# Kernel tuning notes

Measured on AMD Instinct MI355X. Metric: run time of the kernel, lower is better.

The kernel has to match this reference:

```python
import jax, jax.numpy as jnp
import numpy as np

D_MODEL = 5120
NUM_HEADS = 128
HEAD_DIM = D_MODEL // NUM_HEADS  # 40
LATENT = 1536


def setup_inputs() -> dict:
    key = jax.random.key(0)
    ks = jax.random.split(key, 9)
    B, S = 2, 1024
    scale = 0.02
    return {
        "x": jax.random.normal(ks[0], (B, S, D_MODEL), dtype=jnp.float32),
        "Wq": jax.random.normal(ks[1], (D_MODEL, D_MODEL), dtype=jnp.float32) * scale,
        "bq": jnp.zeros((D_MODEL,), dtype=jnp.float32),
        "Wc": jax.random.normal(ks[2], (D_MODEL, LATENT), dtype=jnp.float32) * scale,
        "bc": jnp.zeros((LATENT,), dtype=jnp.float32),
        "Wk": jax.random.normal(ks[3], (LATENT, D_MODEL), dtype=jnp.float32) * scale,
        "bk": jnp.zeros((D_MODEL,), dtype=jnp.float32),
        "Wv": jax.random.normal(ks[4], (LATENT, D_MODEL), dtype=jnp.float32) * scale,
        "bv": jnp.zeros((D_MODEL,), dtype=jnp.float32),
    }


def reference(x, Wq, bq, Wc, bc, Wk, bk, Wv, bv):
    B, S, _ = x.shape
    H, Dh = NUM_HEADS, HEAD_DIM
    # projections
    q = x @ Wq + bq                     # [B,S,D]
    kv_latent = x @ Wc + bc             # [B,S,L]
    k = kv_latent @ Wk + bk             # [B,S,D]
    v = kv_latent @ Wv + bv             # [B,S,D]
    # split heads -> [B,H,S,Dh]
    q = q.reshape(B, S, H, Dh).transpose(0, 2, 1, 3)
    k = k.reshape(B, S, H, Dh).transpose(0, 2, 1, 3)
    v = v.reshape(B, S, H, Dh).transpose(0, 2, 1, 3)
    scores = jnp.einsum("bhqd,bhkd->bhqk", q, k) / jnp.sqrt(jnp.float32(Dh))
    attn = jax.nn.softmax(scores, axis=-1)
    out = jnp.einsum("bhqk,bhkd->bhqd", attn, v)  # [B,H,S,Dh]
    return out.transpose(0, 2, 1, 3).reshape(B, S, H * Dh)
```

## Files before the change

kernel.cpp:

```cpp
#include <hip/hip_runtime.h>
#include <hip/hip_bf16.h>

typedef __attribute__((ext_vector_type(8))) __bf16 bf16x8;
typedef __attribute__((ext_vector_type(4))) __bf16 bf16x4;
typedef __attribute__((ext_vector_type(4))) float f32x4;

#define MFMA16(a, b, c) __builtin_amdgcn_mfma_f32_16x16x32_bf16((a), (b), (c), 0, 0, 0)

#if __has_builtin(__builtin_amdgcn_exp2f)
#define EXP2F(x) __builtin_amdgcn_exp2f(x)
#else
#define EXP2F(x) exp2f(x)
#endif

#define GLDS16(g, l)                                                             \
    __builtin_amdgcn_global_load_lds((const __attribute__((address_space(1))) void*)(g), \
                                     (__attribute__((address_space(3))) void*)(l), 16, 0, 0)

#define BARRIER()                          \
    do {                                   \
        asm volatile("" ::: "memory");     \
        __builtin_amdgcn_s_barrier();      \
        asm volatile("" ::: "memory");     \
    } while (0)

#define WAIT_LGKM0() asm volatile("s_waitcnt lgkmcnt(0)" ::: "memory")
#define VM6 asm volatile("s_waitcnt vmcnt(6)" ::: "memory")
#define VM8 asm volatile("s_waitcnt vmcnt(8)" ::: "memory")
#define VM0 asm volatile("s_waitcnt vmcnt(0)" ::: "memory")
#define VMNONE ((void)0)
#define KEEP(x) x
#define DROP(x)

static __device__ __forceinline__ unsigned short cvt_bf(float f) {
    return __builtin_bit_cast(unsigned short, (__bf16)f);
}

static __device__ __forceinline__ bf16x8 bf8_zero() {
    uint4 z = make_uint4(0, 0, 0, 0);
    return __builtin_bit_cast(bf16x8, z);
}

__global__ __launch_bounds__(256) void prep(const float* __restrict__ X,
                                            const float* __restrict__ Wq,
                                            const float* __restrict__ Wc,
                                            const float* __restrict__ Wk,
                                            const float* __restrict__ Wv,
                                            unsigned short* __restrict__ Xb,
                                            unsigned short* __restrict__ dqc,
                                            unsigned short* __restrict__ dkv) {
    const int D = 5120, L = 1536;
    int b = blockIdx.x, t = threadIdx.x;
    if (b < 5120) {
        int i = (b * 256 + t) * 8;
        float4 f0 = *(const float4*)(X + i);
        float4 f1 = *(const float4*)(X + i + 4);
        unsigned short o[8];
        o[0] = cvt_bf(f0.x); o[1] = cvt_bf(f0.y); o[2] = cvt_bf(f0.z); o[3] = cvt_bf(f0.w);
        o[4] = cvt_bf(f1.x); o[5] = cvt_bf(f1.y); o[6] = cvt_bf(f1.z); o[7] = cvt_bf(f1.w);
        *(uint4*)(Xb + i) = *(const uint4*)o;
        return;
    }
    int b2 = b - 5120;
    const float* W;
    unsigned short* WT;
    int K, N;
    if (b2 < 6400) { W = Wq; WT = dqc; K = D; N = D; }
    else if (b2 < 8320) { b2 -= 6400; W = Wc; WT = dqc + (size_t)D * D; K = D; N = L; }
    else if (b2 < 10240) { b2 -= 8320; W = Wk; WT = dkv; K = L; N = D; }
    else { b2 -= 10240; W = Wv; WT = dkv + (size_t)D * L; K = L; N = D; }
    int nx = N / 64;
    int n0 = (b2 % nx) * 64, k0 = (b2 / nx) * 64;

    __shared__ unsigned short tile[64][65];
    int c4 = (t & 15) * 4, r16 = t >> 4;
#pragma unroll
    for (int it = 0; it < 4; ++it) {
        int r = r16 + it * 16;
        float4 f = *(const float4*)&W[(size_t)(k0 + r) * N + n0 + c4];
        tile[r][c4 + 0] = cvt_bf(f.x);
        tile[r][c4 + 1] = cvt_bf(f.y);
        tile[r][c4 + 2] = cvt_bf(f.z);
        tile[r][c4 + 3] = cvt_bf(f.w);
    }
    __syncthreads();
    int n = t >> 2, kc = (t & 3) * 16;
    unsigned short o[16];
#pragma unroll
    for (int j = 0; j < 16; ++j) o[j] = tile[kc + j][n];
    unsigned short* dst = &WT[(size_t)(n0 + n) * K + k0 + kc];
    *(uint4*)dst = *(const uint4*)o;
    *(uint4*)(dst + 8) = *(const uint4*)(o + 8);
}

__global__ __launch_bounds__(256) void vtrans(const unsigned short* __restrict__ V, int ldv,
                                              unsigned short* __restrict__ VT) {
    int d0 = blockIdx.x * 64, s0 = blockIdx.y * 64;
    __shared__ __align__(16) unsigned short tile[64][72];
    int t = threadIdx.x;
    int r = t >> 3, c8 = (t & 7) * 8;
#pragma unroll
    for (int p = 0; p < 2; ++p) {
        uint4 u = *(const uint4*)&V[(size_t)(s0 + r + p * 32) * ldv + d0 + c8];
        *(uint4*)&tile[r + p * 32][c8] = u;
    }
    __syncthreads();
#pragma unroll
    for (int p = 0; p < 2; ++p) {
        int dr = (t >> 3) + p * 32, cc = (t & 7) * 8;
        unsigned short o[8];
#pragma unroll
        for (int j = 0; j < 8; ++j) o[j] = tile[cc + j][dr];
        *(uint4*)&VT[(size_t)(d0 + dr) * 2048 + s0 + cc] = *(const uint4*)o;
    }
}

#define STAGE_A(S, H, KT)                                                              \
    do {                                                                               \
        GLDS16(aS[H][0] + (size_t)(KT) * 64, &Abuf[S][(H) * 8192 + wid * 512]);        \
        GLDS16(aS[H][1] + (size_t)(KT) * 64, &Abuf[S][(H) * 8192 + 4096 + wid * 512]); \
    } while (0)
#define STAGE_B(S, H, KT)                                                              \
    do {                                                                               \
        GLDS16(bS[H][0] + (size_t)(KT) * 64, &Bbuf[S][(H) * 8192 + wid * 512]);        \
        GLDS16(bS[H][1] + (size_t)(KT) * 64, &Bbuf[S][(H) * 8192 + 4096 + wid * 512]); \
    } while (0)

#define LDA_HALF(S, QM)                                                                   \
    do {                                                                                  \
        _Pragma("unroll") for (int mi = 0; mi < 4; ++mi)                                  \
            _Pragma("unroll") for (int kh = 0; kh < 2; ++kh)                              \
                af[mi][kh] =                                                              \
                    *(const bf16x8*)&Abuf[S][((QM) * 8192 + aoff + mi * 1024) ^ (kh * 32)]; \
    } while (0)
#define LDB_HALF(S, QN, BF)                                                               \
    do {                                                                                  \
        _Pragma("unroll") for (int ni = 0; ni < 2; ++ni)                                  \
            _Pragma("unroll") for (int kh = 0; kh < 2; ++kh)                              \
                BF[ni][kh] =                                                              \
                    *(const bf16x8*)&Bbuf[S][((QN) * 8192 + boff + ni * 1024) ^ (kh * 32)]; \
    } while (0)

#define MMAQ(QM, QN, BF)                                                                \
    do {                                                                                \
        _Pragma("unroll") for (int mi = 0; mi < 4; ++mi)                                \
            _Pragma("unroll") for (int ni = 0; ni < 2; ++ni)                            \
                _Pragma("unroll") for (int kh = 0; kh < 2; ++kh)                        \
                    acc[(QM) * 4 + mi][(QN) * 2 + ni] =                                 \
                        MFMA16(af[mi][kh], BF[ni][kh], acc[(QM) * 4 + mi][(QN) * 2 + ni]); \
    } while (0)

#define KTILE_V2(S, T, STG1, STG2, VMOP, RDNEXT)       \
    {                                                  \
        const int s_ = (S);                            \
        LDB_HALF(s_, 1, bf1);                          \
        STG1(STAGE_B(s_ ^ 1, 0, (T) + 1);)             \
        __builtin_amdgcn_s_setprio(1);                 \
        MMAQ(0, 0, bf0);                               \
        __builtin_amdgcn_s_setprio(0);                 \
        WAIT_LGKM0();                                  \
        BARRIER();                                     \
        STG2(STAGE_A(s_, 0, (T) + 2);                  \
             STAGE_B(s_, 1, (T) + 2);)                 \
        __builtin_amdgcn_s_setprio(1);                 \
        MMAQ(0, 1, bf1);                               \
        __builtin_amdgcn_s_setprio(0);                 \
        LDA_HALF(s_, 1);                               \
        __builtin_amdgcn_s_setprio(1);                 \
        MMAQ(1, 1, bf1);                               \
        __builtin_amdgcn_s_setprio(0);                 \
        WAIT_LGKM0();                                  \
        BARRIER();                                     \
        STG2(STAGE_A(s_, 1, (T) + 2);)                 \
        __builtin_amdgcn_s_setprio(1);                 \
        MMAQ(1, 0, bf0);                               \
        __builtin_amdgcn_s_setprio(0);                 \
        VMOP;                                          \
        BARRIER();                                     \
        RDNEXT(LDA_HALF(s_ ^ 1, 0); LDB_HALF(s_ ^ 1, 0, bf0);) \
    }

__global__ __launch_bounds__(512, 2) void gemm256(const unsigned short* __restrict__ A, int lda,
                                                  const unsigned short* __restrict__ BT, int ldb,
                                                  const float* __restrict__ bias0,
                                                  const float* __restrict__ bias1, int nsplit,
                                                  unsigned short* __restrict__ C, int ldc,
                                                  int K, float s0, float s1, int gx) {
    __shared__ __align__(16) unsigned short Abuf[2][16384];
    __shared__ __align__(16) unsigned short Bbuf[2][16384];

    int nwg = gridDim.x, orig = blockIdx.x;
    int cpx = nwg >> 3;
    int wgid = (orig & 7) * cpx + (orig >> 3);
    int tm = wgid / gx, tn = wgid % gx;
    int m0 = tm * 256, n0 = tn * 256;

    int tid = threadIdx.x, lane = tid & 63, wid = tid >> 6;
    int wm = wid >> 2, wn = wid & 3;
    int lrow = lane & 15, lkg = lane >> 4;

    int t5 = tid >> 3;
    int cole = ((tid & 7) ^ ((tid >> 3) & 7)) << 3;
    const unsigned short* aS[2][2];
    const unsigned short* bS[2][2];
#pragma unroll
    for (int H = 0; H < 2; ++H)
#pragma unroll
        for (int c = 0; c < 2; ++c) {
            int rA = (c << 7) | (H << 6) | t5;
            int rB = (((c << 1) | (t5 >> 5)) << 6) | (H << 5) | (t5 & 31);
            aS[H][c] = A + (size_t)(m0 + rA) * lda + cole;
            bS[H][c] = BT + (size_t)(n0 + rB) * ldb + cole;
        }

    int xorc = (lkg * 8) ^ ((lrow & 7) << 3);
    int aoff = wm * 4096 + lrow * 64 + xorc;
    int boff = wn * 2048 + lrow * 64 + xorc;

    f32x4 acc[8][4];
#pragma unroll
    for (int i = 0; i < 8; ++i)
#pragma unroll
        for (int j = 0; j < 4; ++j) acc[i][j] = (f32x4){0.f, 0.f, 0.f, 0.f};
    bf16x8 af[4][2], bf0[2][2], bf1[2][2];

    const int nkt = K >> 6;

    STAGE_A(0, 0, 0); STAGE_A(0, 1, 0); STAGE_B(0, 0, 0); STAGE_B(0, 1, 0);
    STAGE_A(1, 0, 1); STAGE_B(1, 1, 1); STAGE_A(1, 1, 1);
    VM6;
    BARRIER();
    LDA_HALF(0, 0);
    LDB_HALF(0, 0, bf0);

    int t = 0;
    for (; t + 2 < nkt; ++t) KTILE_V2(t & 1, t, KEEP, KEEP, VM6, KEEP);
    KTILE_V2(t & 1, t, KEEP, DROP, VM0, KEEP);
    ++t;
    KTILE_V2(t & 1, t, DROP, DROP, VMNONE, DROP);

#pragma unroll
    for (int ni = 0; ni < 4; ++ni) {
        int col = n0 + wn * 64 + ni * 16 + lrow;
        float bval = (col < nsplit) ? bias0[col] : bias1[col - nsplit];
        float scl = (col < nsplit) ? s0 : s1;
#pragma unroll
        for (int mi = 0; mi < 8; ++mi) {
            int row = m0 + wm * 128 + mi * 16 + lkg * 4;
#pragma unroll
            for (int j = 0; j < 4; ++j)
                C[(size_t)(row + j) * ldc + col] = cvt_bf((acc[mi][ni][j] + bval) * scl);
        }
    }
}

#define STG128(S, KT)                                                                  \
    do {                                                                               \
        _Pragma("unroll") for (int i_ = 0; i_ < 4; ++i_)                               \
            GLDS16(Ag + (size_t)(i_ * 32) * lda + (size_t)(KT) * 64,                   \
                   &Abuf[S][i_ * 2048 + wid * 512]);                                   \
        _Pragma("unroll") for (int i_ = 0; i_ < 4; ++i_)                               \
            GLDS16(Bg + (size_t)(i_ * 32) * ldb + (size_t)(KT) * 64,                   \
                   &Bbuf[S][i_ * 2048 + wid * 512]);                                   \
    } while (0)

__global__ __launch_bounds__(256, 2) void gemm128(const unsigned short* __restrict__ A, int lda,
                                                  const unsigned short* __restrict__ BT, int ldb,
                                                  const float* __restrict__ bias0,
                                                  const float* __restrict__ bias1, int nsplit,
                                                  unsigned short* __restrict__ C, int ldc,
                                                  int K, float s0, float s1, int gy) {
    __shared__ __align__(16) unsigned short Abuf[2][8192];
    __shared__ __align__(16) unsigned short Bbuf[2][8192];

    int b = blockIdx.x;
    int tm = b % gy, tn = b / gy;
    int m0 = tm * 128, n0 = tn * 128;
    int tid = threadIdx.x, lane = tid & 63, wid = tid >> 6;
    int wm = wid >> 1, wn = wid & 1;
    int lrow = lane & 15, lkg = lane >> 4;

    int srow = tid >> 3;
    int cole = ((tid & 7) ^ ((tid >> 3) & 7)) << 3;
    const unsigned short* Ag = A + (size_t)(m0 + srow) * lda + cole;
    const unsigned short* Bg = BT + (size_t)(n0 + srow) * ldb + cole;

    int xorc8 = (lrow & 7) << 3;
    int aoff = (wm * 64 + lrow) * 64;
    int boff = (wn * 64 + lrow) * 64;

    f32x4 acc[4][4];
#pragma unroll
    for (int i2 = 0; i2 < 4; ++i2)
#pragma unroll
        for (int j = 0; j < 4; ++j) acc[i2][j] = (f32x4){0.f, 0.f, 0.f, 0.f};

    const int nkt = K >> 6;
    STG128(0, 0);
    for (int t = 0; t < nkt; ++t) {
        const int cur = t & 1;
        if (t + 1 < nkt) {
            STG128(cur ^ 1, t + 1);
            VM8;
        } else {
            VM0;
        }
        BARRIER();
        bf16x8 af[4][2], bv[4][2];
#pragma unroll
        for (int mi = 0; mi < 4; ++mi)
#pragma unroll
            for (int kh = 0; kh < 2; ++kh)
                af[mi][kh] = *(const bf16x8*)&Abuf[cur][aoff + mi * 1024 + (((kh * 4 + lkg) << 3) ^ xorc8)];
#pragma unroll
        for (int ni = 0; ni < 4; ++ni)
#pragma unroll
            for (int kh = 0; kh < 2; ++kh)
                bv[ni][kh] = *(const bf16x8*)&Bbuf[cur][boff + ni * 1024 + (((kh * 4 + lkg) << 3) ^ xorc8)];
        __builtin_amdgcn_s_setprio(1);
#pragma unroll
        for (int mi = 0; mi < 4; ++mi)
#pragma unroll
            for (int ni = 0; ni < 4; ++ni)
#pragma unroll
                for (int kh = 0; kh < 2; ++kh)
                    acc[mi][ni] = MFMA16(af[mi][kh], bv[ni][kh], acc[mi][ni]);
        __builtin_amdgcn_s_setprio(0);
        BARRIER();
    }

#pragma unroll
    for (int ni = 0; ni < 4; ++ni) {
        int col = n0 + wn * 64 + ni * 16 + lrow;
        float bval = (col < nsplit) ? bias0[col] : bias1[col - nsplit];
        float scl = (col < nsplit) ? s0 : s1;
#pragma unroll
        for (int mi = 0; mi < 4; ++mi) {
            int row = m0 + wm * 64 + mi * 16 + lkg * 4;
#pragma unroll
            for (int j = 0; j < 4; ++j)
                C[(size_t)(row + j) * ldc + col] = cvt_bf((acc[mi][ni][j] + bval) * scl);
        }
    }
}

__global__ __launch_bounds__(256) void attn(const unsigned short* __restrict__ q, int ldq,
                                            const unsigned short* __restrict__ k, int ldk,
                                            const unsigned short* __restrict__ vT,
                                            float* __restrict__ out) {
    const int S = 1024, D = 5120, Dh = 40;
    int b = blockIdx.z, h = blockIdx.y, qt = blockIdx.x;
    int t = threadIdx.x, lane = t & 63, wid = t >> 6;
    int lrow = lane & 15, lkg = lane >> 4;

    __shared__ __align__(16) unsigned short Ks[64 * 72];
    __shared__ __align__(16) unsigned short Vs[48 * 72];
    __shared__ __align__(16) unsigned short Ps[4][16 * 72];

    const size_t qbase = ((size_t)b * S) * ldq + (size_t)h * Dh;
    int q0 = qt * 64 + wid * 16;

    for (int z = t; z < 8 * 72; z += 256) Vs[40 * 72 + z] = 0;

    bf16x8 qf0, qf1;
    {
        const unsigned short* qp = q + qbase + (size_t)(q0 + lrow) * ldq;
        qf0 = *(const bf16x8*)(qp + lkg * 8);
        qf1 = (lkg == 0) ? *(const bf16x8*)(qp + 32) : bf8_zero();
    }

    int rrK = t >> 3, ccK = t & 7;
    int dV = t >> 3, cV = t & 7;
    const unsigned short* kp = k + ((size_t)b * S) * ldk + (size_t)h * Dh +
                               (size_t)rrK * ldk + ccK * 8;
    const unsigned short* vp = vT + (size_t)(h * Dh + dV) * 2048 + b * S + cV * 8;
    const unsigned short* vp2 = vT + (size_t)(h * Dh + 32 + dV) * 2048 + b * S + cV * 8;
    const size_t kstep = (size_t)64 * ldk;

    uint4 kv0, kv1, va0, va1;
    kv0 = kv1 = va0 = va1 = make_uint4(0, 0, 0, 0);
    if (ccK < 5) { kv0 = *(const uint4*)kp; kv1 = *(const uint4*)(kp + 32 * ldk); }
    va0 = *(const uint4*)vp;
    if (t < 64) va1 = *(const uint4*)vp2;
    kp += kstep; vp += 64; vp2 += 64;

    f32x4 acc[3];
#pragma unroll
    for (int nb = 0; nb < 3; ++nb) acc[nb] = (f32x4){0.f, 0.f, 0.f, 0.f};
    float mrun = -INFINITY, lrun = 0.f;

    for (int kt = 0; kt < 16; ++kt) {
        __syncthreads();
        uint4 w0 = (ccK < 5) ? kv0 : make_uint4(0, 0, 0, 0);
        uint4 w1 = (ccK < 5) ? kv1 : make_uint4(0, 0, 0, 0);
        *(uint4*)&Ks[rrK * 72 + ccK * 8] = w0;
        *(uint4*)&Ks[(rrK + 32) * 72 + ccK * 8] = w1;
        *(uint4*)&Vs[dV * 72 + cV * 8] = va0;
        if (t < 64) *(uint4*)&Vs[(32 + dV) * 72 + cV * 8] = va1;
        __syncthreads();
        if (kt + 1 < 16) {
            if (ccK < 5) { kv0 = *(const uint4*)kp; kv1 = *(const uint4*)(kp + 32 * ldk); }
            va0 = *(const uint4*)vp;
            if (t < 64) va1 = *(const uint4*)vp2;
            kp += kstep; vp += 64; vp2 += 64;
        }

        f32x4 sf[4];
        __builtin_amdgcn_s_setprio(1);
#pragma unroll
        for (int nb = 0; nb < 4; ++nb) {
            sf[nb] = (f32x4){0.f, 0.f, 0.f, 0.f};
            bf16x8 kf0 = *(const bf16x8*)&Ks[(nb * 16 + lrow) * 72 + lkg * 8];
            bf16x8 kf1 = *(const bf16x8*)&Ks[(nb * 16 + lrow) * 72 + 32 + lkg * 8];
            sf[nb] = MFMA16(kf0, qf0, sf[nb]);
            sf[nb] = MFMA16(kf1, qf1, sf[nb]);
        }
        __builtin_amdgcn_s_setprio(0);

        float tm = sf[0][0];
#pragma unroll
        for (int nb = 0; nb < 4; ++nb)
#pragma unroll
            for (int i = 0; i < 4; ++i) tm = fmaxf(tm, sf[nb][i]);
        tm = fmaxf(tm, __shfl_xor(tm, 16));
        tm = fmaxf(tm, __shfl_xor(tm, 32));

        float mn = mrun, al = 1.0f;
        bool resc = !__all(tm <= mrun + 11.0f);
        if (resc) {
            mn = fmaxf(mrun, tm);
            al = EXP2F(mrun - mn);
            mrun = mn;
        }
        float rs = 0.f;
#pragma unroll
        for (int nb = 0; nb < 4; ++nb) {
            bf16x4 pk;
#pragma unroll
            for (int i = 0; i < 4; ++i) {
                float p = EXP2F(sf[nb][i] - mn);
                rs += p;
                pk[i] = (__bf16)p;
            }
            *(bf16x4*)&Ps[wid][lrow * 72 + nb * 16 + lkg * 4] = pk;
        }
        rs += __shfl_xor(rs, 16);
        rs += __shfl_xor(rs, 32);
        lrun = lrun * al + rs;

        if (resc) {
            float alr[4];
#pragma unroll
            for (int i = 0; i < 4; ++i) alr[i] = __shfl(al, lkg * 4 + i);
#pragma unroll
            for (int nb = 0; nb < 3; ++nb)
#pragma unroll
                for (int i = 0; i < 4; ++i) acc[nb][i] *= alr[i];
        }

        __builtin_amdgcn_s_setprio(1);
#pragma unroll
        for (int kk = 0; kk < 2; ++kk) {
            bf16x8 pf = *(const bf16x8*)&Ps[wid][lrow * 72 + kk * 32 + lkg * 8];
#pragma unroll
            for (int nb = 0; nb < 3; ++nb) {
                bf16x8 vf = *(const bf16x8*)&Vs[(nb * 16 + lrow) * 72 + kk * 32 + lkg * 8];
                acc[nb] = MFMA16(pf, vf, acc[nb]);
            }
        }
        __builtin_amdgcn_s_setprio(0);
    }

    float lr[4];
#pragma unroll
    for (int i = 0; i < 4; ++i) lr[i] = __shfl(lrun, lkg * 4 + i);
#pragma unroll
    for (int i = 0; i < 4; ++i) {
        float inv = 1.0f / lr[i];
        int s = q0 + lkg * 4 + i;
#pragma unroll
        for (int nb = 0; nb < 3; ++nb) {
            int d = nb * 16 + lrow;
            if (d < Dh) out[((size_t)(b * S + s)) * D + h * Dh + d] = acc[nb][i] * inv;
        }
    }
}

extern "C" void kernel_launch(void* const* d_in, const int* in_sizes, int n_in,
                              void* d_out, int out_size, void* d_ws, size_t ws_size,
                              hipStream_t stream) {
    const int M = 2048, D = 5120, L = 1536, NQ = D + L , NKV = 2 * D ;
    const float* x  = (const float*)d_in[0];
    const float* Wq = (const float*)d_in[1];
    const float* bq = (const float*)d_in[2];
    const float* Wc = (const float*)d_in[3];
    const float* bc = (const float*)d_in[4];
    const float* Wk = (const float*)d_in[5];
    const float* bk = (const float*)d_in[6];
    const float* Wv = (const float*)d_in[7];
    const float* bv = (const float*)d_in[8];
    float* out = (float*)d_out;

    unsigned short* ws = (unsigned short*)d_ws;
    size_t off = 0;
    unsigned short* xb    = ws + off; off += (size_t)M * D;
    unsigned short* WqcT  = ws + off; off += (size_t)NQ * D;
    unsigned short* WkvT  = ws + off; off += (size_t)NKV * L;
    unsigned short* qkvb  = ws + off; off += (size_t)M * NQ;
    unsigned short* kvout = ws + off; off += (size_t)M * NKV;
    unsigned short* vTb   = ws + off; off += (size_t)D * M;

    prep<<<17280, 256, 0, stream>>>(x, Wq, Wc, Wk, Wv, xb, WqcT, WkvT);

    const float qscale = 1.4426950408889634f / 6.324555320336759f;

    gemm256<<<dim3((NQ / 256) * (M / 256)), 512, 0, stream>>>(xb, D, WqcT, D, bq, bc, D,
                                                              qkvb, NQ, D, qscale, 1.0f,
                                                              NQ / 256);
    gemm128<<<dim3((NKV / 128) * (M / 128)), 256, 0, stream>>>(qkvb + D, NQ, WkvT, L, bk, bv, D,
                                                               kvout, NKV, L, 1.0f, 1.0f,
                                                               M / 128);
    vtrans<<<dim3(D / 64, M / 64), 256, 0, stream>>>(kvout + D, NKV, vTb);

    attn<<<dim3(1024 / 64, 128, 2), 256, 0, stream>>>(qkvb, NQ, kvout, NKV, vTb, out);
}
```

Before: 457.4 us.

## Fuse V transpose into KV GEMM epilogue and process two query tiles per warp

The KV projection GEMM now writes the V half of its output directly in transposed layout, so the separate vtrans kernel and its extra round trip through global memory are gone. The attention kernel has each wave handle 32 query rows (two 16-row groups) instead of 16, halving the grid and reusing each staged K/V tile for twice as many queries. The cost is higher register pressure in attention and fewer blocks to spread across the GPU. The transposed epilogue stores are 8-byte writes strided by 2048 elements, which may coalesce poorly.

```diff
diff --git a/kernel.cpp b/kernel.cpp
--- a/kernel.cpp
+++ b/kernel.cpp
@@ -91,28 +91,6 @@
     unsigned short* dst = &WT[(size_t)(n0 + n) * K + k0 + kc];
     *(uint4*)dst = *(const uint4*)o;
     *(uint4*)(dst + 8) = *(const uint4*)(o + 8);
-}
-
-__global__ __launch_bounds__(256) void vtrans(const unsigned short* __restrict__ V, int ldv,
-                                              unsigned short* __restrict__ VT) {
-    int d0 = blockIdx.x * 64, s0 = blockIdx.y * 64;
-    __shared__ __align__(16) unsigned short tile[64][72];
-    int t = threadIdx.x;
-    int r = t >> 3, c8 = (t & 7) * 8;
-#pragma unroll
-    for (int p = 0; p < 2; ++p) {
-        uint4 u = *(const uint4*)&V[(size_t)(s0 + r + p * 32) * ldv + d0 + c8];
-        *(uint4*)&tile[r + p * 32][c8] = u;
-    }
-    __syncthreads();
-#pragma unroll
-    for (int p = 0; p < 2; ++p) {
-        int dr = (t >> 3) + p * 32, cc = (t & 7) * 8;
-        unsigned short o[8];
-#pragma unroll
-        for (int j = 0; j < 8; ++j) o[j] = tile[cc + j][dr];
-        *(uint4*)&VT[(size_t)(d0 + dr) * 2048 + s0 + cc] = *(const uint4*)o;
-    }
 }
 
 #define STAGE_A(S, H, KT)                                                              \
@@ -269,7 +247,8 @@
                                                   const float* __restrict__ bias0,
                                                   const float* __restrict__ bias1, int nsplit,
                                                   unsigned short* __restrict__ C, int ldc,
-                                                  int K, float s0, float s1, int gy) {
+                                                  unsigned short* __restrict__ VT,
+                                                  int K, int gy) {
     __shared__ __align__(16) unsigned short Abuf[2][8192];
     __shared__ __align__(16) unsigned short Bbuf[2][8192];
 
@@ -333,13 +312,21 @@
     for (int ni = 0; ni < 4; ++ni) {
         int col = n0 + wn * 64 + ni * 16 + lrow;
         float bval = (col < nsplit) ? bias0[col] : bias1[col - nsplit];
-        float scl = (col < nsplit) ? s0 : s1;
 #pragma unroll
         for (int mi = 0; mi < 4; ++mi) {
             int row = m0 + wm * 64 + mi * 16 + lkg * 4;
-#pragma unroll
-            for (int j = 0; j < 4; ++j)
-                C[(size_t)(row + j) * ldc + col] = cvt_bf((acc[mi][ni][j] + bval) * scl);
+            if (col < nsplit) {
+#pragma unroll
+                for (int j = 0; j < 4; ++j)
+                    C[(size_t)(row + j) * ldc + col] = cvt_bf(acc[mi][ni][j] + bval);
+            } else {
+                ushort4 o;
+                o.x = cvt_bf(acc[mi][ni][0] + bval);
+                o.y = cvt_bf(acc[mi][ni][1] + bval);
+                o.z = cvt_bf(acc[mi][ni][2] + bval);
+                o.w = cvt_bf(acc[mi][ni][3] + bval);
+                *(ushort4*)&VT[(size_t)(col - nsplit) * 2048 + row] = o;
+            }
         }
     }
 }
@@ -358,15 +345,16 @@
     __shared__ __align__(16) unsigned short Ps[4][16 * 72];
 
     const size_t qbase = ((size_t)b * S) * ldq + (size_t)h * Dh;
-    int q0 = qt * 64 + wid * 16;
+    int q0 = qt * 128 + wid * 32;
 
     for (int z = t; z < 8 * 72; z += 256) Vs[40 * 72 + z] = 0;
 
-    bf16x8 qf0, qf1;
-    {
-        const unsigned short* qp = q + qbase + (size_t)(q0 + lrow) * ldq;
-        qf0 = *(const bf16x8*)(qp + lkg * 8);
-        qf1 = (lkg == 0) ? *(const bf16x8*)(qp + 32) : bf8_zero();
+    bf16x8 qf[2][2];
+#pragma unroll
+    for (int g = 0; g < 2; ++g) {
+        const unsigned short* qp = q + qbase + (size_t)(q0 + g * 16 + lrow) * ldq;
+        qf[g][0] = *(const bf16x8*)(qp + lkg * 8);
+        qf[g][1] = (lkg == 0) ? *(const bf16x8*)(qp + 32) : bf8_zero();
     }
 
     int rrK = t >> 3, ccK = t & 7;
@@ -384,10 +372,12 @@
     if (t < 64) va1 = *(const uint4*)vp2;
     kp += kstep; vp += 64; vp2 += 64;
 
-    f32x4 acc[3];
-#pragma unroll
-    for (int nb = 0; nb < 3; ++nb) acc[nb] = (f32x4){0.f, 0.f, 0.f, 0.f};
-    float mrun = -INFINITY, lrun = 0.f;
+    f32x4 acc[2][3];
+#pragma unroll
+    for (int g = 0; g < 2; ++g)
+#pragma unroll
+        for (int nb = 0; nb < 3; ++nb) acc[g][nb] = (f32x4){0.f, 0.f, 0.f, 0.f};
+    float mrun[2] = {-INFINITY, -INFINITY}, lrun[2] = {0.f, 0.f};
 
     for (int kt = 0; kt < 16; ++kt) {
         __syncthreads();
@@ -405,83 +395,89 @@
             kp += kstep; vp += 64; vp2 += 64;
         }
 
-        f32x4 sf[4];
-        __builtin_amdgcn_s_setprio(1);
-#pragma unroll
-        for (int nb = 0; nb < 4; ++nb) {
-            sf[nb] = (f32x4){0.f, 0.f, 0.f, 0.f};
-            bf16x8 kf0 = *(const bf16x8*)&Ks[(nb * 16 + lrow) * 72 + lkg * 8];
-            bf16x8 kf1 = *(const bf16x8*)&Ks[(nb * 16 + lrow) * 72 + 32 + lkg * 8];
-            sf[nb] = MFMA16(kf0, qf0, sf[nb]);
-            sf[nb] = MFMA16(kf1, qf1, sf[nb]);
-        }
-        __builtin_amdgcn_s_setprio(0);
-
-        float tm = sf[0][0];
-#pragma unroll
-        for (int nb = 0; nb < 4; ++nb)
-#pragma unroll
-            for (int i = 0; i < 4; ++i) tm = fmaxf(tm, sf[nb][i]);
-        tm = fmaxf(tm, __shfl_xor(tm, 16));
-        tm = fmaxf(tm, __shfl_xor(tm, 32));
-
-        float mn = mrun, al = 1.0f;
-        bool resc = !__all(tm <= mrun + 11.0f);
-        if (resc) {
-            mn = fmaxf(mrun, tm);
-            al = EXP2F(mrun - mn);
-            mrun = mn;
-        }
-        float rs = 0.f;
-#pragma unroll
-        for (int nb = 0; nb < 4; ++nb) {
-            bf16x4 pk;
-#pragma unroll
-            for (int i = 0; i < 4; ++i) {
-                float p = EXP2F(sf[nb][i] - mn);
-                rs += p;
-                pk[i] = (__bf16)p;
-            }
-            *(bf16x4*)&Ps[wid][lrow * 72 + nb * 16 + lkg * 4] = pk;
-        }
-        rs += __shfl_xor(rs, 16);
-        rs += __shfl_xor(rs, 32);
-        lrun = lrun * al + rs;
-
-        if (resc) {
-            float alr[4];
-#pragma unroll
-            for (int i = 0; i < 4; ++i) alr[i] = __shfl(al, lkg * 4 + i);
-#pragma unroll
-            for (int nb = 0; nb < 3; ++nb)
-#pragma unroll
-                for (int i = 0; i < 4; ++i) acc[nb][i] *= alr[i];
-        }
-
-        __builtin_amdgcn_s_setprio(1);
-#pragma unroll
-        for (int kk = 0; kk < 2; ++kk) {
-            bf16x8 pf = *(const bf16x8*)&Ps[wid][lrow * 72 + kk * 32 + lkg * 8];
+#pragma unroll
+        for (int g = 0; g < 2; ++g) {
+            f32x4 sf[4];
+            __builtin_amdgcn_s_setprio(1);
+#pragma unroll
+            for (int nb = 0; nb < 4; ++nb) {
+                sf[nb] = (f32x4){0.f, 0.f, 0.f, 0.f};
+                bf16x8 kf0 = *(const bf16x8*)&Ks[(nb * 16 + lrow) * 72 + lkg * 8];
+                bf16x8 kf1 = *(const bf16x8*)&Ks[(nb * 16 + lrow) * 72 + 32 + lkg * 8];
+                sf[nb] = MFMA16(kf0, qf[g][0], sf[nb]);
+                sf[nb] = MFMA16(kf1, qf[g][1], sf[nb]);
+            }
+            __builtin_amdgcn_s_setprio(0);
+
+            float tm = sf[0][0];
+#pragma unroll
+            for (int nb = 0; nb < 4; ++nb)
+#pragma unroll
+                for (int i = 0; i < 4; ++i) tm = fmaxf(tm, sf[nb][i]);
+            tm = fmaxf(tm, __shfl_xor(tm, 16));
+            tm = fmaxf(tm, __shfl_xor(tm, 32));
+
+            float mn = mrun[g], al = 1.0f;
+            bool resc = !__all(tm <= mrun[g] + 11.0f);
+            if (resc) {
+                mn = fmaxf(mrun[g], tm);
+                al = EXP2F(mrun[g] - mn);
+                mrun[g] = mn;
+            }
+            float rs = 0.f;
+#pragma unroll
+            for (int nb = 0; nb < 4; ++nb) {
+                bf16x4 pk;
+#pragma unroll
+                for (int i = 0; i < 4; ++i) {
+                    float p = EXP2F(sf[nb][i] - mn);
+                    rs += p;
+                    pk[i] = (__bf16)p;
+                }
+                *(bf16x4*)&Ps[wid][lrow * 72 + nb * 16 + lkg * 4] = pk;
+            }
+            rs += __shfl_xor(rs, 16);
+            rs += __shfl_xor(rs, 32);
+            lrun[g] = lrun[g] * al + rs;
+
+            if (resc) {
+                float alr[4];
+#pragma unroll
+                for (int i = 0; i < 4; ++i) alr[i] = __shfl(al, lkg * 4 + i);
+#pragma unroll
+                for (int nb = 0; nb < 3; ++nb)
+#pragma unroll
+                    for (int i = 0; i < 4; ++i) acc[g][nb][i] *= alr[i];
+            }
+
+            __builtin_amdgcn_s_setprio(1);
+#pragma unroll
+            for (int kk = 0; kk < 2; ++kk) {
+                bf16x8 pf = *(const bf16x8*)&Ps[wid][lrow * 72 + kk * 32 + lkg * 8];
+#pragma unroll
+                for (int nb = 0; nb < 3; ++nb) {
+                    bf16x8 vf = *(const bf16x8*)&Vs[(nb * 16 + lrow) * 72 + kk * 32 + lkg * 8];
+                    acc[g][nb] = MFMA16(pf, vf, acc[g][nb]);
+                }
+            }
+            __builtin_amdgcn_s_setprio(0);
+        }
+    }
+
+#pragma unroll
+    for (int g = 0; g < 2; ++g) {
+        float lr[4];
+#pragma unroll
+        for (int i = 0; i < 4; ++i) lr[i] = __shfl(lrun[g], lkg * 4 + i);
+#pragma unroll
+        for (int i = 0; i < 4; ++i) {
+            float inv = 1.0f / lr[i];
+            int s = q0 + g * 16 + lkg * 4 + i;
 #pragma unroll
             for (int nb = 0; nb < 3; ++nb) {
-                bf16x8 vf = *(const bf16x8*)&Vs[(nb * 16 + lrow) * 72 + kk * 32 + lkg * 8];
-                acc[nb] = MFMA16(pf, vf, acc[nb]);
-            }
-        }
-        __builtin_amdgcn_s_setprio(0);
-    }
-
-    float lr[4];
-#pragma unroll
-    for (int i = 0; i < 4; ++i) lr[i] = __shfl(lrun, lkg * 4 + i);
-#pragma unroll
-    for (int i = 0; i < 4; ++i) {
-        float inv = 1.0f / lr[i];
-        int s = q0 + lkg * 4 + i;
-#pragma unroll
-        for (int nb = 0; nb < 3; ++nb) {
-            int d = nb * 16 + lrow;
-            if (d < Dh) out[((size_t)(b * S + s)) * D + h * Dh + d] = acc[nb][i] * inv;
+                int d = nb * 16 + lrow;
+                if (d < Dh) out[((size_t)(b * S + s)) * D + h * Dh + d] = acc[g][nb][i] * inv;
+            }
         }
     }
 }
@@ -518,9 +514,7 @@
                                                               qkvb, NQ, D, qscale, 1.0f,
                                                               NQ / 256);
     gemm128<<<dim3((NKV / 128) * (M / 128)), 256, 0, stream>>>(qkvb + D, NQ, WkvT, L, bk, bv, D,
-                                                               kvout, NKV, L, 1.0f, 1.0f,
-                                                               M / 128);
-    vtrans<<<dim3(D / 64, M / 64), 256, 0, stream>>>(kvout + D, NKV, vTb);
-
-    attn<<<dim3(1024 / 64, 128, 2), 256, 0, stream>>>(qkvb, NQ, kvout, NKV, vTb, out);
-}
+                                                               kvout, NKV, vTb, L, M / 128);
+
+    attn<<<dim3(1024 / 128, 128, 2), 256, 0, stream>>>(qkvb, NQ, kvout, NKV, vTb, out);
+}
```

After: 445.1 us. -2.7%, faster.
